# Optimization experiments

Hardware: AMD Instinct MI355X
Metric: run time of the kernel (lower is better)

## Reference

```python
import jax, jax.numpy as jnp
import numpy as np

B, S, E = 2, 2048, 2048
H = 16
KV_RANK = 512
ROPE = 64
NOPE = 64  # source sets qk_nope_dim = qk_rope_dim
VD = 128   # v_head_dim = head_dim
QD = ROPE + NOPE  # q_head_dim = 128


def setup_inputs() -> dict:
    key = jax.random.key(0)
    ks = jax.random.split(key, 5)
    sd = lambda fan_in: 1.0 / np.sqrt(fan_in)
    return {
        "x": jax.random.normal(ks[0], (B, S, E), jnp.float32),
        "attention_mask": jnp.zeros((1, 1, S, S), jnp.float32),
        "W_kv_down": jax.random.normal(ks[1], (KV_RANK + ROPE, E), jnp.float32) * sd(E),
        "W_kv_up": jax.random.normal(ks[2], (H * (VD + NOPE), KV_RANK), jnp.float32) * sd(KV_RANK),
        "W_q": jax.random.normal(ks[3], (H * QD, E), jnp.float32) * sd(E),
        "W_out": jax.random.normal(ks[4], (E, H * VD), jnp.float32) * sd(H * VD),
    }


def reference(x, attention_mask, W_kv_down, W_kv_up, W_q, W_out):
    scale = QD ** (-0.5)
    # down-project to latent + rope part
    compressed = jnp.einsum('bse,fe->bsf', x, W_kv_down)          # [B,S,KV_RANK+ROPE]
    kv_c, k_rope = compressed[..., :KV_RANK], compressed[..., KV_RANK:]
    # up-project latent to per-head v and k_nope
    kv_exp = jnp.einsum('bsr,fr->bsf', kv_c, W_kv_up)             # [B,S,H*(VD+NOPE)]
    kv_exp = kv_exp.reshape(B, S, H, VD + NOPE).transpose(0, 2, 1, 3)  # [B,H,S,VD+NOPE]
    v, k_nope = kv_exp[..., :VD], kv_exp[..., VD:]
    # shared rope key broadcast over heads, concat [rope, nope]
    k_rope_b = jnp.broadcast_to(k_rope[:, None], (B, H, S, ROPE))
    k = jnp.concatenate([k_rope_b, k_nope], axis=-1)              # [B,H,S,QD]
    # queries
    q = jnp.einsum('bse,fe->bsf', x, W_q).reshape(B, S, H, QD).transpose(0, 2, 1, 3)
    scores = jnp.einsum('bhsd,bhtd->bhst', q, k) * scale + attention_mask
    w = jax.nn.softmax(scores, axis=-1)
    out = jnp.einsum('bhst,bhtv->bhsv', w, v)                     # [B,H,S,VD]
    out = out.transpose(0, 2, 1, 3).reshape(B, S, H * VD)
    return jnp.einsum('bsf,ef->bse', out, W_out)
```

## Files before the change

kernel.cpp:

```cpp
#include <hip/hip_runtime.h>
#include <hip/hip_bf16.h>
#include <stdint.h>

typedef __bf16 bf16x8 __attribute__((ext_vector_type(8)));
typedef float f32x4 __attribute__((ext_vector_type(4)));
typedef float f32x16 __attribute__((ext_vector_type(16)));
typedef uint32_t u32x4 __attribute__((ext_vector_type(4)));
typedef unsigned short ushort_t;
typedef unsigned short ushort8v __attribute__((ext_vector_type(8)));

#define MFMA16 __builtin_amdgcn_mfma_f32_16x16x32_bf16
#define MFMA32 __builtin_amdgcn_mfma_f32_32x32x16_bf16

static constexpr int Bc = 2, Sc = 2048, Ec = 2048, Hc = 16;

__device__ __forceinline__ void gload16(const void* g, void* l) {
  __builtin_amdgcn_global_load_lds(
      (const __attribute__((address_space(1))) void*)g,
      (__attribute__((address_space(3))) void*)l, 16, 0, 0);
}

__device__ __forceinline__ ushort_t f2bf(float f) {
  uint32_t u = __float_as_uint(f);
  uint32_t r = (u + 0x7fffu + ((u >> 16) & 1u)) >> 16;
  return (ushort_t)r;
}
__device__ __forceinline__ float bf2f(ushort_t u) {
  return __uint_as_float((uint32_t)u << 16);
}
__device__ __forceinline__ uint32_t cvtpk(float a, float b) {
  uint32_t d;
  asm("v_cvt_pk_bf16_f32 %0, %1, %2" : "=v"(d) : "v"(a), "v"(b));
  return d;
}
__device__ __forceinline__ void plswap(uint32_t& a, uint32_t& b) {
  asm("v_permlane32_swap_b32 %0, %1" : "+v"(a), "+v"(b));
}

__global__ void cast_all(const float* __restrict__ x, const float* __restrict__ Wq,
                         const float* __restrict__ Wkvu, const float* __restrict__ Wout,
                         const float* __restrict__ Wkvd,
                         ushort_t* __restrict__ xb, ushort_t* __restrict__ wq,
                         ushort_t* __restrict__ wkvu, ushort_t* __restrict__ wout,
                         ushort_t* __restrict__ wkvd) {
  int i = blockIdx.x * 256 + threadIdx.x;
  const float* src;
  ushort_t* dst;
  int j;
  if (i < 2097152) { src = x; dst = xb; j = i; }
  else if (i < 3145728) { src = Wq; dst = wq; j = i - 2097152; }
  else if (i < 3538944) { src = Wkvu; dst = wkvu; j = i - 3145728; }
  else if (i < 4587520) { src = Wout; dst = wout; j = i - 3538944; }
  else {
    j = i - 4587520;
    int row = j >> 9, col4 = j & 511;
    ushort4 o;
    if (row < 576) {
      float4 v = ((const float4*)Wkvd)[row * 512 + col4];
      o.x = f2bf(v.x); o.y = f2bf(v.y); o.z = f2bf(v.z); o.w = f2bf(v.w);
    } else { o.x = 0; o.y = 0; o.z = 0; o.w = 0; }
    ((ushort4*)wkvd)[j] = o;
    return;
  }
  float4 v = ((const float4*)src)[j];
  ushort4 o;
  o.x = f2bf(v.x); o.y = f2bf(v.y); o.z = f2bf(v.z); o.w = f2bf(v.w);
  ((ushort4*)dst)[j] = o;
}

__global__ void mask_rearrange(const float* __restrict__ mask, ushort_t* __restrict__ m4) {
  const float INVLN2 = 1.4426950408889634f;
  int i = blockIdx.x * 256 + threadIdx.x;
  if (i >= 524288) return;
  int rr = i & 1, half = (i >> 1) & 1, kblk = (i >> 2) & 1, kt = (i >> 3) & 31, q = i >> 8;
  const float* src = mask + (size_t)q * 2048 + kt * 64 + kblk * 32 + half * 4 + rr * 16;
  float4 a = *(const float4*)src;
  float4 c = *(const float4*)(src + 8);
  ushort8v o;
  o[0] = f2bf(a.x * INVLN2); o[1] = f2bf(a.y * INVLN2);
  o[2] = f2bf(a.z * INVLN2); o[3] = f2bf(a.w * INVLN2);
  o[4] = f2bf(c.x * INVLN2); o[5] = f2bf(c.y * INVLN2);
  o[6] = f2bf(c.z * INVLN2); o[7] = f2bf(c.w * INVLN2);
  ((ushort8v*)m4)[i] = o;
}

template<int MODE>
__global__ __launch_bounds__(256, 2)
void gemm_bt(const ushort_t* __restrict__ A, int lda,
             const ushort_t* __restrict__ Bm, int ldb,
             void* __restrict__ Cout, int ldc,
             int M, int N, int K,
             char* __restrict__ vtb, char* __restrict__ kbuf)
{
  __shared__ __align__(16) ushort_t sA[2][128 * 32];
  __shared__ __align__(16) ushort_t sB[2][128 * 32];
  int tid = threadIdx.x;
  int nTn = N >> 7;
  int bid = blockIdx.x;
  int chunk = gridDim.x >> 3;
  bid = (bid & 7) * chunk + (bid >> 3);
  int tm = bid / nTn, tn = bid - tm * nTn;
  int wave = tid >> 6, lane = tid & 63;
  int wm = (wave >> 1) << 6, wn = (wave & 1) << 6;
  int l16 = lane & 15, g16 = lane >> 4;
  f32x4 acc[4][4] = {};
  int srow = tid >> 2, scol = (tid & 3) << 3;
  const ushort_t* Ag = A + (size_t)(tm * 128 + srow) * lda + scol;
  const ushort_t* Bg = Bm + (size_t)(tn * 128 + srow) * ldb + scol;
  ushort_t* sA0 = &sA[0][srow * 32 + scol];
  ushort_t* sA1 = &sA[1][srow * 32 + scol];
  ushort_t* sB0 = &sB[0][srow * 32 + scol];
  ushort_t* sB1 = &sB[1][srow * 32 + scol];
  for (int kt = 0; kt < K; kt += 64) {
    gload16(Ag, sA0);
    gload16(Ag + (size_t)64 * lda, sA0 + 64 * 32);
    gload16(Ag + 32, sA1);
    gload16(Ag + (size_t)64 * lda + 32, sA1 + 64 * 32);
    gload16(Bg, sB0);
    gload16(Bg + (size_t)64 * ldb, sB0 + 64 * 32);
    gload16(Bg + 32, sB1);
    gload16(Bg + (size_t)64 * ldb + 32, sB1 + 64 * 32);
    Ag += 64; Bg += 64;
    __syncthreads();
#pragma unroll
    for (int h2 = 0; h2 < 2; h2++) {
      bf16x8 af[4], bfr[4];
#pragma unroll
      for (int i = 0; i < 4; i++) af[i] = *(const bf16x8*)&sA[h2][(wm + i * 16 + l16) * 32 + g16 * 8];
#pragma unroll
      for (int i = 0; i < 4; i++) bfr[i] = *(const bf16x8*)&sB[h2][(wn + i * 16 + l16) * 32 + g16 * 8];
#pragma unroll
      for (int i = 0; i < 4; i++)
#pragma unroll
        for (int j = 0; j < 4; j++)
          acc[i][j] = MFMA16(af[i], bfr[j], acc[i][j], 0, 0, 0);
    }
    __syncthreads();
  }
#pragma unroll
  for (int i = 0; i < 4; i++) {
#pragma unroll
    for (int j = 0; j < 4; j++) {
      int grow0 = tm * 128 + wm + i * 16 + g16 * 4;
      int gcol = tn * 128 + wn + j * 16 + l16;
      if constexpr (MODE == 0) {
#pragma unroll
        for (int r = 0; r < 4; r++)
          ((ushort_t*)Cout)[(size_t)(grow0 + r) * ldc + gcol] = f2bf(acc[i][j][r]);
      } else if constexpr (MODE == 2) {
#pragma unroll
        for (int r = 0; r < 4; r++)
          ((float*)Cout)[(size_t)(grow0 + r) * ldc + gcol] = acc[i][j][r];
      } else {
        int h = gcol / 192, jj = gcol - h * 192;
        int b = grow0 >> 11, s0 = grow0 & 2047;
        size_t bh = (size_t)(b * Hc + h);
        if (jj < 128) {
          ushort4 pk;
          pk.x = f2bf(acc[i][j][0]); pk.y = f2bf(acc[i][j][1]);
          pk.z = f2bf(acc[i][j][2]); pk.w = f2bf(acc[i][j][3]);
          *(ushort4*)(vtb + bh * 524288 + (size_t)jj * 4096 + ((s0 >> 6) * 128) +
                      ((2 * (s0 & 63)) ^ ((jj & 7) << 4))) = pk;
        } else {
          int col = 64 + (jj - 128);
#pragma unroll
          for (int r = 0; r < 4; r++) {
            int s = s0 + r;
            *(ushort_t*)(kbuf + (bh * Sc + s) * 256 + ((2 * col) ^ ((s & 7) << 4))) = f2bf(acc[i][j][r]);
          }
        }
      }
    }
  }
}

__global__ void rope_fill(const ushort_t* __restrict__ comp, char* __restrict__ kbuf) {
  int i = blockIdx.x * 256 + threadIdx.x;
  if (i >= Bc * Sc * 8) return;
  int blk = i & 7;
  int m = i >> 3;
  int s = m & 2047, b = m >> 11;
  uint4 v = *(const uint4*)&comp[(size_t)m * 640 + 512 + blk * 8];
  int off = (blk * 16) ^ ((s & 7) << 4);
#pragma unroll
  for (int h = 0; h < Hc; h++) {
    *(uint4*)(kbuf + ((size_t)(b * Hc + h) * Sc + s) * 256 + off) = v;
  }
}

__global__ __launch_bounds__(128, 2)
void attn_kernel(const ushort_t* __restrict__ qb, const char* __restrict__ kbuf,
                 const char* __restrict__ vtb, const ushort_t* __restrict__ m4,
                 ushort_t* __restrict__ attn_o)
{
  __shared__ __align__(16) char smem[32768];
  char* sK = smem;
  char* sV = smem + 16384;
  const float scale2 = 0.12752081738040466f;
  int bid = blockIdx.x;
  bid = (bid & 7) * 128 + (bid >> 3);
  int qt = bid & 31, bh = bid >> 5;
  int b = bh >> 4, h = bh & 15;
  int tid = threadIdx.x, wave = tid >> 6, lane = tid & 63;
  int l32 = lane & 31, half = lane >> 5;
  int sx = (l32 & 7) << 4;
  int qbase = qt * 64 + wave * 32;

  bf16x8 qf[8];
  {
    const ushort_t* qp = qb + (size_t)(b * Sc + qbase + l32) * 2048 + h * 128 + half * 8;
#pragma unroll
    for (int ks = 0; ks < 8; ks++) qf[ks] = *(const bf16x8*)(qp + ks * 16);
  }

  float mrun = -3.0e38f, lrun = 0.f;
  f32x16 acco[4] = {};

  const char* kg = kbuf + (size_t)bh * 524288;
  const char* vg = vtb + (size_t)bh * 524288;
  const ushort8v* mq = (const ushort8v*)m4 + (size_t)(qbase + l32) * 256 + half * 2;

  for (int kt = 0; kt < 32; kt++) {
#pragma unroll
    for (int it = 0; it < 8; it++)
      gload16(kg + kt * 16384 + it * 2048 + tid * 16, sK + it * 2048 + tid * 16);
#pragma unroll
    for (int it = 0; it < 8; it++) {
      int l = it * 2048 + tid * 16;
      gload16(vg + (size_t)(l >> 7) * 4096 + kt * 128 + (l & 127), sV + l);
    }
    ushort8v mvv[4];
#pragma unroll
    for (int kb = 0; kb < 2; kb++)
#pragma unroll
      for (int rr = 0; rr < 2; rr++)
        mvv[kb * 2 + rr] = mq[kt * 8 + kb * 4 + rr];
    __syncthreads();

#pragma unroll
    for (int kblk = 0; kblk < 2; kblk++) {
      f32x16 sc = {};
      __builtin_amdgcn_s_setprio(1);
#pragma unroll
      for (int ks = 0; ks < 8; ks++) {
        bf16x8 kfr = *(const bf16x8*)(sK + (kblk * 32 + l32) * 256 +
                                      ((ks * 32 + half * 16) ^ sx));
        sc = MFMA32(kfr, qf[ks], sc, 0, 0, 0);
      }
      __builtin_amdgcn_s_setprio(0);

#pragma unroll
      for (int r = 0; r < 16; r++)
        sc[r] = sc[r] * scale2 + bf2f(mvv[kblk * 2 + (r >> 3)][r & 7]);
      float mx = sc[0];
#pragma unroll
      for (int r = 1; r < 16; r++) mx = fmaxf(mx, sc[r]);
      mx = fmaxf(mx, __shfl_xor(mx, 32));
      if (!__all(mx <= mrun + 11.0f)) {
        float mnew = fmaxf(mrun, mx);
        float corr = __builtin_amdgcn_exp2f(mrun - mnew);
        lrun *= corr; mrun = mnew;
#pragma unroll
        for (int r = 0; r < 16; r++) {
          float cr = __shfl(corr, (r & 3) + 8 * (r >> 2) + 4 * half);
#pragma unroll
          for (int vb = 0; vb < 4; vb++) acco[vb][r] *= cr;
        }
      }
      float rs = 0.f;
      uint32_t W[8];
#pragma unroll
      for (int m = 0; m < 4; m++) {
        float p0 = __builtin_amdgcn_exp2f(sc[4 * m + 0] - mrun);
        float p1 = __builtin_amdgcn_exp2f(sc[4 * m + 1] - mrun);
        float p2 = __builtin_amdgcn_exp2f(sc[4 * m + 2] - mrun);
        float p3 = __builtin_amdgcn_exp2f(sc[4 * m + 3] - mrun);
        rs += (p0 + p1) + (p2 + p3);
        W[2 * m] = cvtpk(p0, p1);
        W[2 * m + 1] = cvtpk(p2, p3);
      }
      lrun += rs;

      bf16x8 pf[2];
#pragma unroll
      for (int k2 = 0; k2 < 2; k2++) {
        uint32_t a0 = W[4 * k2 + 0], a1 = W[4 * k2 + 1];
        uint32_t b0 = W[4 * k2 + 2], b1 = W[4 * k2 + 3];
        plswap(a0, b0);
        plswap(a1, b1);
        u32x4 t; t[0] = a0; t[1] = a1; t[2] = b0; t[3] = b1;
        pf[k2] = __builtin_bit_cast(bf16x8, t);
      }

      __builtin_amdgcn_s_setprio(1);
#pragma unroll
      for (int k2 = 0; k2 < 2; k2++)
#pragma unroll
        for (int vb = 0; vb < 4; vb++) {
          bf16x8 vf = *(const bf16x8*)(sV + (vb * 32 + l32) * 128 +
                                       ((kblk * 64 + k2 * 32 + half * 16) ^ sx));
          acco[vb] = MFMA32(pf[k2], vf, acco[vb], 0, 0, 0);
        }
      __builtin_amdgcn_s_setprio(0);
    }

    __syncthreads();
  }

  lrun += __shfl_xor(lrun, 32);
#pragma unroll
  for (int r = 0; r < 16; r++) {
    int rowq = (r & 3) + 8 * (r >> 2) + 4 * half;
    float lr = __shfl(lrun, rowq);
    float inv = 1.0f / lr;
    int qrow = qbase + rowq;
    ushort_t* op = attn_o + (size_t)(b * Sc + qrow) * 2048 + h * 128 + l32;
#pragma unroll
    for (int vb = 0; vb < 4; vb++)
      op[vb * 32] = f2bf(acco[vb][r] * inv);
  }
}

extern "C" void kernel_launch(void* const* d_in, const int* in_sizes, int n_in,
                              void* d_out, int out_size, void* d_ws, size_t ws_size,
                              hipStream_t stream) {
  const float* x    = (const float*)d_in[0];
  const float* mask = (const float*)d_in[1];
  const float* Wkvd = (const float*)d_in[2];
  const float* Wkvu = (const float*)d_in[3];
  const float* Wq   = (const float*)d_in[4];
  const float* Wout = (const float*)d_in[5];

  char* ws = (char*)d_ws;
  size_t off = 0;
  auto alloc = [&](size_t bytes) { char* p = ws + off; off += (bytes + 255) & ~(size_t)255; return p; };
  ushort_t* xb   = (ushort_t*)alloc((size_t)4096 * 2048 * 2);
  ushort_t* wkvd = (ushort_t*)alloc((size_t)640 * 2048 * 2);
  ushort_t* wq   = (ushort_t*)alloc((size_t)2048 * 2048 * 2);
  ushort_t* wkvu = (ushort_t*)alloc((size_t)3072 * 512 * 2);
  ushort_t* wout = (ushort_t*)alloc((size_t)2048 * 2048 * 2);
  ushort_t* comp = (ushort_t*)alloc((size_t)4096 * 640 * 2);
  ushort_t* qbuf = (ushort_t*)alloc((size_t)4096 * 2048 * 2);
  char*     kbuf = alloc((size_t)Bc * Hc * Sc * 256);
  char*     vtb  = alloc((size_t)Bc * Hc * 524288);
  ushort_t* attn_o = xb;
  ushort_t* m4 = wq;

  cast_all<<<19200, 256, 0, stream>>>(x, Wq, Wkvu, Wout, Wkvd, xb, wq, wkvu, wout, wkvd);

  gemm_bt<0><<<32 * 5, 256, 0, stream>>>(xb, 2048, wkvd, 2048, comp, 640, 4096, 640, 2048, nullptr, nullptr);
  gemm_bt<0><<<32 * 16, 256, 0, stream>>>(xb, 2048, wq, 2048, qbuf, 2048, 4096, 2048, 2048, nullptr, nullptr);
  mask_rearrange<<<2048, 256, 0, stream>>>(mask, m4);
  gemm_bt<1><<<32 * 24, 256, 0, stream>>>(comp, 640, wkvu, 512, nullptr, 0, 4096, 3072, 512, vtb, kbuf);
  rope_fill<<<32768 / 256, 256, 0, stream>>>(comp, kbuf);
  attn_kernel<<<1024, 128, 0, stream>>>(qbuf, kbuf, vtb, m4, attn_o);
  gemm_bt<2><<<32 * 16, 256, 0, stream>>>(attn_o, 2048, wout, 2048, d_out, 2048, 4096, 2048, 2048, nullptr, nullptr);
}
```

Before: 263.0 us.

## Use 256x256-tile GEMM kernel for Q and output projections; merge mask and rope prep

Adds a new GEMM kernel with 256x256 output tiles, 512 threads, a K-step of 64 and s_setprio around the MFMA bursts. It is used for the Q projection and the output projection in place of the 128x128 gemm_bt, aiming for more data reuse per LDS load and fewer global loads. The mask rearrangement and the rope broadcast fill are merged into one prep kernel, saving a launch. Only 128 blocks are launched on a chip with 256 CUs, so half the CUs may sit idle. The prep kernel now writes the rope part of kbuf before gemm_bt<1> writes the nope columns, which is safe only because the two touch disjoint columns.

```diff
diff --git a/kernel.cpp b/kernel.cpp
--- a/kernel.cpp
+++ b/kernel.cpp
@@ -68,20 +68,34 @@
   ((ushort4*)dst)[j] = o;
 }
 
-__global__ void mask_rearrange(const float* __restrict__ mask, ushort_t* __restrict__ m4) {
+__global__ void prep_kernel(const float* __restrict__ mask, ushort_t* __restrict__ m4,
+                            const ushort_t* __restrict__ comp, char* __restrict__ kbuf) {
   const float INVLN2 = 1.4426950408889634f;
-  int i = blockIdx.x * 256 + threadIdx.x;
-  if (i >= 524288) return;
-  int rr = i & 1, half = (i >> 1) & 1, kblk = (i >> 2) & 1, kt = (i >> 3) & 31, q = i >> 8;
-  const float* src = mask + (size_t)q * 2048 + kt * 64 + kblk * 32 + half * 4 + rr * 16;
-  float4 a = *(const float4*)src;
-  float4 c = *(const float4*)(src + 8);
-  ushort8v o;
-  o[0] = f2bf(a.x * INVLN2); o[1] = f2bf(a.y * INVLN2);
-  o[2] = f2bf(a.z * INVLN2); o[3] = f2bf(a.w * INVLN2);
-  o[4] = f2bf(c.x * INVLN2); o[5] = f2bf(c.y * INVLN2);
-  o[6] = f2bf(c.z * INVLN2); o[7] = f2bf(c.w * INVLN2);
-  ((ushort8v*)m4)[i] = o;
+  int gb = blockIdx.x;
+  if (gb < 2048) {
+    int i = gb * 256 + threadIdx.x;
+    int rr = i & 1, half = (i >> 1) & 1, kblk = (i >> 2) & 1, kt = (i >> 3) & 31, q = i >> 8;
+    const float* src = mask + (size_t)q * 2048 + kt * 64 + kblk * 32 + half * 4 + rr * 16;
+    float4 a = *(const float4*)src;
+    float4 c = *(const float4*)(src + 8);
+    ushort8v o;
+    o[0] = f2bf(a.x * INVLN2); o[1] = f2bf(a.y * INVLN2);
+    o[2] = f2bf(a.z * INVLN2); o[3] = f2bf(a.w * INVLN2);
+    o[4] = f2bf(c.x * INVLN2); o[5] = f2bf(c.y * INVLN2);
+    o[6] = f2bf(c.z * INVLN2); o[7] = f2bf(c.w * INVLN2);
+    ((ushort8v*)m4)[i] = o;
+  } else {
+    int i = (gb - 2048) * 256 + threadIdx.x;
+    int blk = i & 7;
+    int m = i >> 3;
+    int s = m & 2047, b = m >> 11;
+    uint4 v = *(const uint4*)&comp[(size_t)m * 640 + 512 + blk * 8];
+    int off = (blk * 16) ^ ((s & 7) << 4);
+#pragma unroll
+    for (int h = 0; h < Hc; h++) {
+      *(uint4*)(kbuf + ((size_t)(b * Hc + h) * Sc + s) * 256 + off) = v;
+    }
+  }
 }
 
 template<int MODE>
@@ -147,10 +161,6 @@
 #pragma unroll
         for (int r = 0; r < 4; r++)
           ((ushort_t*)Cout)[(size_t)(grow0 + r) * ldc + gcol] = f2bf(acc[i][j][r]);
-      } else if constexpr (MODE == 2) {
-#pragma unroll
-        for (int r = 0; r < 4; r++)
-          ((float*)Cout)[(size_t)(grow0 + r) * ldc + gcol] = acc[i][j][r];
       } else {
         int h = gcol / 192, jj = gcol - h * 192;
         int b = grow0 >> 11, s0 = grow0 & 2047;
@@ -174,17 +184,83 @@
   }
 }
 
-__global__ void rope_fill(const ushort_t* __restrict__ comp, char* __restrict__ kbuf) {
-  int i = blockIdx.x * 256 + threadIdx.x;
-  if (i >= Bc * Sc * 8) return;
-  int blk = i & 7;
-  int m = i >> 3;
-  int s = m & 2047, b = m >> 11;
-  uint4 v = *(const uint4*)&comp[(size_t)m * 640 + 512 + blk * 8];
-  int off = (blk * 16) ^ ((s & 7) << 4);
-#pragma unroll
-  for (int h = 0; h < Hc; h++) {
-    *(uint4*)(kbuf + ((size_t)(b * Hc + h) * Sc + s) * 256 + off) = v;
+template<int OUTF>
+__global__ __launch_bounds__(512, 2)
+void gemm256(const ushort_t* __restrict__ A, const ushort_t* __restrict__ Bm,
+             void* __restrict__ Cout, int M, int N, int K)
+{
+  __shared__ __align__(16) ushort_t sA[2][256 * 64];
+  __shared__ __align__(16) ushort_t sB[2][256 * 64];
+  int tid = threadIdx.x;
+  int nTn = N >> 8;
+  int bid = blockIdx.x;
+  int chunk = gridDim.x >> 3;
+  bid = (bid & 7) * chunk + (bid >> 3);
+  int tm = bid / nTn, tn = bid - tm * nTn;
+  int wave = tid >> 6, lane = tid & 63;
+  int wm = wave >> 2, wn = wave & 3;
+  int l16 = lane & 15, g16 = lane >> 4;
+  f32x4 acc[8][4] = {};
+
+  int srow0 = tid >> 3;
+  int colsw = ((tid & 7) ^ (srow0 & 7)) * 8;
+  const ushort_t* Ag = A + (size_t)(tm * 256 + srow0) * K + colsw;
+  const ushort_t* Bg = Bm + (size_t)(tn * 256 + srow0) * K + colsw;
+
+  auto ISSUE = [&](int kk, int nb) {
+#pragma unroll
+    for (int it = 0; it < 4; it++) {
+      gload16(Ag + (size_t)(it * 64) * K + kk, (char*)sA[nb] + it * 8192 + tid * 16);
+      gload16(Bg + (size_t)(it * 64) * K + kk, (char*)sB[nb] + it * 8192 + tid * 16);
+    }
+  };
+
+  ISSUE(0, 0);
+  int Kt = K >> 6;
+  int csw = (l16 & 7) << 4;
+  for (int kt = 0; kt < Kt; kt++) {
+    int buf = kt & 1;
+    __syncthreads();
+    if (kt + 1 < Kt) ISSUE((kt + 1) * 64, buf ^ 1);
+    const char* bA = (const char*)sA[buf];
+    const char* bB = (const char*)sB[buf];
+#pragma unroll
+    for (int ks = 0; ks < 2; ks++) {
+      int c = (ks * 64 + g16 * 16) ^ csw;
+      bf16x8 bf[4];
+#pragma unroll
+      for (int j = 0; j < 4; j++)
+        bf[j] = *(const bf16x8*)(bB + (wn * 64 + j * 16 + l16) * 128 + c);
+#pragma unroll
+      for (int mh = 0; mh < 2; mh++) {
+        bf16x8 af[4];
+#pragma unroll
+        for (int i = 0; i < 4; i++)
+          af[i] = *(const bf16x8*)(bA + (wm * 128 + mh * 64 + i * 16 + l16) * 128 + c);
+        __builtin_amdgcn_s_setprio(1);
+#pragma unroll
+        for (int i = 0; i < 4; i++)
+#pragma unroll
+          for (int j = 0; j < 4; j++)
+            acc[mh * 4 + i][j] = MFMA16(af[i], bf[j], acc[mh * 4 + i][j], 0, 0, 0);
+        __builtin_amdgcn_s_setprio(0);
+      }
+    }
+  }
+#pragma unroll
+  for (int mi = 0; mi < 8; mi++) {
+#pragma unroll
+    for (int j = 0; j < 4; j++) {
+      int grow0 = tm * 256 + wm * 128 + mi * 16 + g16 * 4;
+      int gcol = tn * 256 + wn * 64 + j * 16 + l16;
+#pragma unroll
+      for (int r = 0; r < 4; r++) {
+        if constexpr (OUTF == 0)
+          ((ushort_t*)Cout)[(size_t)(grow0 + r) * N + gcol] = f2bf(acc[mi][j][r]);
+        else
+          ((float*)Cout)[(size_t)(grow0 + r) * N + gcol] = acc[mi][j][r];
+      }
+    }
   }
 }
 
@@ -349,10 +425,9 @@
   cast_all<<<19200, 256, 0, stream>>>(x, Wq, Wkvu, Wout, Wkvd, xb, wq, wkvu, wout, wkvd);
 
   gemm_bt<0><<<32 * 5, 256, 0, stream>>>(xb, 2048, wkvd, 2048, comp, 640, 4096, 640, 2048, nullptr, nullptr);
-  gemm_bt<0><<<32 * 16, 256, 0, stream>>>(xb, 2048, wq, 2048, qbuf, 2048, 4096, 2048, 2048, nullptr, nullptr);
-  mask_rearrange<<<2048, 256, 0, stream>>>(mask, m4);
+  gemm256<0><<<128, 512, 0, stream>>>(xb, wq, qbuf, 4096, 2048, 2048);
+  prep_kernel<<<2176, 256, 0, stream>>>(mask, m4, comp, kbuf);
   gemm_bt<1><<<32 * 24, 256, 0, stream>>>(comp, 640, wkvu, 512, nullptr, 0, 4096, 3072, 512, vtb, kbuf);
-  rope_fill<<<32768 / 256, 256, 0, stream>>>(comp, kbuf);
   attn_kernel<<<1024, 128, 0, stream>>>(qbuf, kbuf, vtb, m4, attn_o);
-  gemm_bt<2><<<32 * 16, 256, 0, stream>>>(attn_o, 2048, wout, 2048, d_out, 2048, 4096, 2048, 2048, nullptr, nullptr);
-}
+  gemm256<2><<<128, 512, 0, stream>>>(attn_o, wout, d_out, 4096, 2048, 2048);
+}
```

New measurement: 306.3 us. 16.4% more time.
